# Kernel tuning notes

Hardware: AMD Instinct MI355X
Metric: run time of the kernel (lower is better)

Reference implementation:

```python
import jax, jax.numpy as jnp
import numpy as np

B, C, L, O = 32, 256, 336, 96
K, NLAYERS, DFF = 4, 2, 1024
EPS = 1e-5


def setup_inputs() -> dict:
    key = jax.random.key(0)
    ks = jax.random.split(key, 10)
    s1 = 1.0 / np.sqrt(L)
    s2 = 1.0 / np.sqrt(DFF)
    return {
        "x": jax.random.normal(ks[0], (B, C, L), dtype=jnp.float32),
        "rev_w": jnp.ones((C,), dtype=jnp.float32),
        "rev_b": jnp.zeros((C,), dtype=jnp.float32),
        "W1": jax.random.normal(ks[1], (K, NLAYERS, L, DFF), dtype=jnp.float32) * s1,
        "b1": jnp.zeros((K, NLAYERS, DFF), dtype=jnp.float32),
        "W2": jax.random.normal(ks[2], (K, NLAYERS, DFF, L), dtype=jnp.float32) * s2,
        "b2": jnp.zeros((K, NLAYERS, L), dtype=jnp.float32),
        "Wh": jax.random.normal(ks[3], (K, L, O), dtype=jnp.float32) * s1,
        "bh": jnp.zeros((K, O), dtype=jnp.float32),
        "assign": jax.random.randint(ks[4], (C,), 0, K, dtype=jnp.int32),
    }


def reference(x, rev_w, rev_b, W1, b1, W2, b2, Wh, bh, assign):
    # RevIN norm over the time axis, per instance and per channel. x: [B,C,L]
    mean = jnp.mean(x, axis=-1, keepdims=True)
    std = jnp.sqrt(jnp.var(x, axis=-1, keepdims=True) + EPS)
    xn = (x - mean) / std * rev_w[None, :, None] + rev_b[None, :, None]

    n_clusters = Wh.shape[0]
    n_layers = W1.shape[1]
    out = jnp.zeros(x.shape[:2] + (Wh.shape[-1],), dtype=x.dtype)  # [B,C,O]
    for k in range(n_clusters):
        z = xn  # [B,C,L] time-mixing MLP stack shared across channels
        for l in range(n_layers):
            h = jax.nn.relu(jnp.einsum('bcl,ld->bcd', z, W1[k, l]) + b1[k, l])
            z = z + jnp.einsum('bcd,dl->bcl', h, W2[k, l]) + b2[k, l]
        y = jnp.einsum('bcl,lo->bco', z, Wh[k]) + bh[k]  # [B,C,O]
        out = jnp.where((assign == k)[None, :, None], y, out)

    # RevIN denorm, then transpose to [B, out_len, C]
    out = (out - rev_b[None, :, None]) / rev_w[None, :, None] * std + mean
    return jnp.transpose(out, (0, 2, 1))
```

## Files before the change

kernel.cpp:

```cpp
#include <hip/hip_runtime.h>
#include <math.h>


typedef unsigned short u16;
typedef unsigned int u32;
typedef unsigned long long u64;

constexpr int B = 32, C = 256, L = 336, O = 96, K = 4, NL = 2, DFF = 1024;
constexpr int TM = 32;
constexpr int NTILES = (B * C) / TM;
constexpr int LP = 352;
constexpr int KS1 = LP / 32;
constexpr int KS2 = DFF / 32;
constexpr int NT2 = LP / 16;
constexpr int NTH = O / 16;
constexpr int ZBS = 360;
constexpr int HS = 1032;

constexpr int W1FRAGS = (DFF / 16) * KS1 * 64;
constexpr int W2FRAGS = NT2 * KS2 * 64;
constexpr int WHFRAGS = NTH * KS1 * 64;
constexpr int NW1 = W1FRAGS * K * NL;
constexpr int NW2 = W2FRAGS * K * NL;

typedef __bf16 bf16x8 __attribute__((ext_vector_type(8)));
typedef float f32x4 __attribute__((ext_vector_type(4)));

__device__ __forceinline__ u16 f2bf(float f) {
  union { float f; u32 u; } v;
  v.f = f;
  u32 r = v.u + 0x7fffu + ((v.u >> 16) & 1u);
  return (u16)(r >> 16);
}
__device__ __forceinline__ float bf2f(u16 h) {
  union { u32 u; float f; } v;
  v.u = ((u32)h) << 16;
  return v.f;
}
__device__ __forceinline__ u32 pack2(float a, float b) {
  return (u32)f2bf(a) | ((u32)f2bf(b) << 16);
}

__global__ __launch_bounds__(256) void build_tables(
    const int* __restrict__ assign, int* __restrict__ meta) {
  __shared__ int wcnt[4][K];
  __shared__ int pre[4][K];
  __shared__ int cofs[K + 1];
  const int tid = threadIdx.x;
  const int w = tid >> 6, lane = tid & 63;
  const int a = assign[tid];
  const u64 below = (1ull << lane) - 1ull;
  int myrank = 0;
#pragma unroll
  for (int k = 0; k < K; ++k) {
    const u64 m = __ballot(a == k);
    if (a == k) myrank = (int)__popcll(m & below);
    if (lane == 0) wcnt[w][k] = (int)__popcll(m);
  }
  __syncthreads();
  if (tid == 0) {
    int tot[K];
    for (int k = 0; k < K; ++k) {
      int s = 0;
      for (int ww = 0; ww < 4; ++ww) {
        pre[ww][k] = s;
        s += wcnt[ww][k];
      }
      tot[k] = s;
    }
    cofs[0] = 0;
    for (int k = 0; k < K; ++k) cofs[k + 1] = cofs[k] + tot[k];
    for (int k = 0; k <= K; ++k) meta[512 + k] = cofs[k];
  }
  __syncthreads();
  const int pos = cofs[a] + pre[w][a] + myrank;
  meta[256 + pos] = tid;
  int k = 0;
  while (k < K - 1 && tid >= cofs[k + 1]) ++k;
  meta[tid] = (k << 16) | ((tid - cofs[k]) * TM);
}


__global__ __launch_bounds__(256) void repack_w1(const float* __restrict__ W1,
                                                 u16* __restrict__ wbuf) {
  __shared__ u16 sm[32][516];
  const int tid = threadIdx.x;
  const int wid = tid >> 6, lane = tid & 63;
  const int dh = blockIdx.x & 1;
  const int ks = (blockIdx.x >> 1) % 11;
  const int kl = blockIdx.x / 22;
  for (int rr = 0; rr < 8; ++rr) {
    const int r = wid * 8 + rr;
    const int l = ks * 32 + r;
#pragma unroll
    for (int h = 0; h < 2; ++h) {
      const int c = h * 256 + lane * 4;
      float4 v = make_float4(0.f, 0.f, 0.f, 0.f);
      if (l < L)
        v = *(const float4*)(W1 + ((size_t)kl * L + l) * DFF + dh * 512 + c);
      uint2 p;
      p.x = pack2(v.x, v.y);
      p.y = pack2(v.z, v.w);
      *(uint2*)&sm[r][c] = p;
    }
  }
  __syncthreads();
  const int q = lane >> 4, rm = lane & 15;
  for (int e = 0; e < 8; ++e) {
    const int ntl = wid * 8 + e;
    const int nt = dh * 32 + ntl;
    uint4 o;
    u32 w4[4];
#pragma unroll
    for (int jj = 0; jj < 4; ++jj) {
      const u16 a = sm[q * 8 + 2 * jj][ntl * 16 + rm];
      const u16 b = sm[q * 8 + 2 * jj + 1][ntl * 16 + rm];
      w4[jj] = (u32)a | ((u32)b << 16);
    }
    o.x = w4[0]; o.y = w4[1]; o.z = w4[2]; o.w = w4[3];
    *(uint4*)(wbuf + ((size_t)(kl * 64 + nt) * 11 + ks) * 512 + lane * 8) = o;
  }
}

__global__ __launch_bounds__(256) void repack_w2(const float* __restrict__ W2,
                                                 u16* __restrict__ wbuf) {
  __shared__ u16 sm[32][356];
  const int tid = threadIdx.x;
  const int wid = tid >> 6, lane = tid & 63;
  const int ks = blockIdx.x & 31;
  const int kl = blockIdx.x >> 5;
  for (int rr = 0; rr < 8; ++rr) {
    const int r = wid * 8 + rr;
    const float* row = W2 + ((size_t)kl * DFF + ks * 32 + r) * L;
    {
      const int c = lane * 4;
      const float4 v = *(const float4*)(row + c);
      uint2 p;
      p.x = pack2(v.x, v.y);
      p.y = pack2(v.z, v.w);
      *(uint2*)&sm[r][c] = p;
    }
    {
      const int c = 256 + lane * 4;
      if (c < 352) {
        float4 v = make_float4(0.f, 0.f, 0.f, 0.f);
        if (c < L) v = *(const float4*)(row + c);
        uint2 p;
        p.x = pack2(v.x, v.y);
        p.y = pack2(v.z, v.w);
        *(uint2*)&sm[r][c] = p;
      }
    }
  }
  __syncthreads();
  const int q = lane >> 4, rm = lane & 15;
  for (int nt = wid; nt < NT2; nt += 4) {
    u32 w4[4];
#pragma unroll
    for (int jj = 0; jj < 4; ++jj) {
      const u16 a = sm[q * 8 + 2 * jj][nt * 16 + rm];
      const u16 b = sm[q * 8 + 2 * jj + 1][nt * 16 + rm];
      w4[jj] = (u32)a | ((u32)b << 16);
    }
    uint4 o;
    o.x = w4[0]; o.y = w4[1]; o.z = w4[2]; o.w = w4[3];
    *(uint4*)(wbuf + (size_t)NW1 * 8 +
              ((size_t)(kl * 22 + nt) * 32 + ks) * 512 + lane * 8) = o;
  }
}

__global__ __launch_bounds__(256) void repack_wh(const float* __restrict__ Wh,
                                                 u16* __restrict__ wbuf) {
  __shared__ u16 sm[32][100];
  const int tid = threadIdx.x;
  const int wid = tid >> 6, lane = tid & 63;
  const int ks = blockIdx.x % 11;
  const int kk = blockIdx.x / 11;
  for (int rr = 0; rr < 8; ++rr) {
    const int r = wid * 8 + rr;
    const int l = ks * 32 + r;
    if (lane < 24) {
      const int c = lane * 4;
      float4 v = make_float4(0.f, 0.f, 0.f, 0.f);
      if (l < L) v = *(const float4*)(Wh + ((size_t)kk * L + l) * O + c);
      uint2 p;
      p.x = pack2(v.x, v.y);
      p.y = pack2(v.z, v.w);
      *(uint2*)&sm[r][c] = p;
    }
  }
  __syncthreads();
  const int q = lane >> 4, rm = lane & 15;
  for (int nt = wid; nt < NTH; nt += 4) {
    u32 w4[4];
#pragma unroll
    for (int jj = 0; jj < 4; ++jj) {
      const u16 a = sm[q * 8 + 2 * jj][nt * 16 + rm];
      const u16 b = sm[q * 8 + 2 * jj + 1][nt * 16 + rm];
      w4[jj] = (u32)a | ((u32)b << 16);
    }
    uint4 o;
    o.x = w4[0]; o.y = w4[1]; o.z = w4[2]; o.w = w4[3];
    *(uint4*)(wbuf + (size_t)(NW1 + NW2) * 8 +
              ((size_t)(kk * 6 + nt) * 11 + ks) * 512 + lane * 8) = o;
  }
}

__global__ __launch_bounds__(512, 2) void mlp_mfma(
    const float* __restrict__ x, const float* __restrict__ rev_w,
    const float* __restrict__ rev_b, const float* __restrict__ b1,
    const float* __restrict__ b2, const float* __restrict__ bh,
    const int* __restrict__ meta, const u16* __restrict__ wbuf,
    float* __restrict__ out) {
  __shared__ __align__(16) u16 zb[TM][ZBS];
  __shared__ __align__(16) u16 Hsh[TM][HS];
  __shared__ float s_mean[TM], s_std[TM], s_rw[TM], s_rb[TM];
  __shared__ int s_b[TM], s_c[TM];

  const int tid = threadIdx.x;
  const int wid = tid >> 6;
  const int lane = tid & 63;
  const int q = lane >> 4, rm = lane & 15;

  const int swz = (blockIdx.x & 7) * 32 + (blockIdx.x >> 3);
  const int info = meta[swz];
  const int kcl = info >> 16;
  const int rstart = info & 0xffff;
  const int cofs = meta[512 + kcl];
  const int cnt = meta[512 + kcl + 1] - cofs;

  for (int i = 0; i < 4; ++i) {
    const int t = wid * 4 + i;
    const int ri = rstart + t;
    const int b = ri / cnt;
    const int c = meta[256 + cofs + (ri % cnt)];
    const float* xrow = x + (size_t)(b * C + c) * L;
    float v[6], s = 0.f, s2 = 0.f;
#pragma unroll
    for (int jj = 0; jj < 6; ++jj) {
      const int j = lane + jj * 64;
      v[jj] = (j < L) ? xrow[j] : 0.f;
      s += v[jj];
      s2 += v[jj] * v[jj];
    }
#pragma unroll
    for (int off = 32; off > 0; off >>= 1) {
      s += __shfl_down(s, off);
      s2 += __shfl_down(s2, off);
    }
    s = __shfl(s, 0);
    s2 = __shfl(s2, 0);
    const float mean = s * (1.f / L);
    const float var = s2 * (1.f / L) - mean * mean;
    const float stdv = sqrtf(var + 1e-5f);
    const float rstd = 1.f / stdv;
    const float rw = rev_w[c], rb_ = rev_b[c];
#pragma unroll
    for (int jj = 0; jj < 6; ++jj) {
      const int j = lane + jj * 64;
      if (j < L) zb[t][j] = f2bf((v[jj] - mean) * rstd * rw + rb_);
    }
    if (lane < LP - L) zb[t][L + lane] = 0;
    if (lane == 0) {
      s_mean[t] = mean;
      s_std[t] = stdv;
      s_rw[t] = rw;
      s_rb[t] = rb_;
      s_b[t] = b;
      s_c[t] = c;
    }
  }

  const u16* w1b = wbuf;
  const u16* w2b = wbuf + (size_t)NW1 * 8;
  const u16* whb = wbuf + (size_t)(NW1 + NW2) * 8;
  constexpr int TS1 = KS1 * 512;
  constexpr int TS2 = KS2 * 512;

  bf16x8 acur[8], anxt[8];
  {
    const u16* base =
        w1b + (size_t)(kcl * NL) * W1FRAGS * 8 + (size_t)(wid * 8) * TS1 + lane * 8;
#pragma unroll
    for (int t = 0; t < 8; ++t) {
      acur[t] = *(const bf16x8*)(base + (size_t)t * TS1);
      anxt[t] = *(const bf16x8*)(base + (size_t)t * TS1 + 512);
    }
  }
  __syncthreads();

  f32x4 zm[3][2];
#pragma unroll
  for (int t = 0; t < 3; ++t) {
    const int nt2 = wid + 8 * t;
#pragma unroll
    for (int rg = 0; rg < 2; ++rg) {
      if (nt2 < NT2) {
        const uint2 zw = *(const uint2*)&zb[rm + 16 * rg][nt2 * 16 + q * 4];
        zm[t][rg] = f32x4{bf2f((u16)zw.x), bf2f((u16)(zw.x >> 16)),
                          bf2f((u16)zw.y), bf2f((u16)(zw.y >> 16))};
      } else {
        zm[t][rg] = f32x4{0.f, 0.f, 0.f, 0.f};
      }
    }
  }

  for (int l = 0; l < NL; ++l) {
    const int kl = kcl * NL + l;
    const u16* W1f = w1b + (size_t)kl * W1FRAGS * 8;
    const u16* W2f = w2b + (size_t)kl * W2FRAGS * 8;
    const float* b1p = b1 + kl * DFF;
    const float* b2p = b2 + kl * L;
    const u16* base1 = W1f + (size_t)(wid * 8) * TS1 + lane * 8;

    f32x4 acc[8][2];
#pragma unroll
    for (int t = 0; t < 8; ++t)
#pragma unroll
      for (int rg = 0; rg < 2; ++rg) acc[t][rg] = f32x4{0.f, 0.f, 0.f, 0.f};
#pragma unroll 2
    for (int ks = 0; ks < KS1; ++ks) {
      bf16x8 ause[8];
#pragma unroll
      for (int t = 0; t < 8; ++t) {
        ause[t] = acur[t];
        acur[t] = anxt[t];
      }
      if (ks + 2 < KS1) {
#pragma unroll
        for (int t = 0; t < 8; ++t)
          anxt[t] = *(const bf16x8*)(base1 + (size_t)t * TS1 + (ks + 2) * 512);
      }
      const bf16x8 zf0 = *(const bf16x8*)&zb[rm][ks * 32 + q * 8];
      const bf16x8 zf1 = *(const bf16x8*)&zb[rm + 16][ks * 32 + q * 8];
#pragma unroll
      for (int t = 0; t < 8; ++t) {
        acc[t][0] =
            __builtin_amdgcn_mfma_f32_16x16x32_bf16(ause[t], zf0, acc[t][0], 0, 0, 0);
        acc[t][1] =
            __builtin_amdgcn_mfma_f32_16x16x32_bf16(ause[t], zf1, acc[t][1], 0, 0, 0);
      }
    }
#pragma unroll
    for (int t = 0; t < 8; ++t) {
      const int nt = wid * 8 + t;
      const float4 bq = *(const float4*)(b1p + nt * 16 + q * 4);
#pragma unroll
      for (int rg = 0; rg < 2; ++rg) {
        uint2 hw;
        hw.x = pack2(fmaxf(acc[t][rg][0] + bq.x, 0.f),
                     fmaxf(acc[t][rg][1] + bq.y, 0.f));
        hw.y = pack2(fmaxf(acc[t][rg][2] + bq.z, 0.f),
                     fmaxf(acc[t][rg][3] + bq.w, 0.f));
        *(uint2*)&Hsh[rm + 16 * rg][nt * 16 + q * 4] = hw;
      }
    }

    const u16* base2 = W2f + lane * 8;
    bf16x8 wq0[3], wq1[3], wq2[3];
#pragma unroll
    for (int t = 0; t < 3; ++t) {
      const int nt2 = wid + 8 * t;
      if (nt2 < NT2) {
        wq0[t] = *(const bf16x8*)(base2 + (size_t)nt2 * TS2);
        wq1[t] = *(const bf16x8*)(base2 + (size_t)nt2 * TS2 + 512);
        wq2[t] = *(const bf16x8*)(base2 + (size_t)nt2 * TS2 + 1024);
      }
    }
    __syncthreads();

#pragma unroll 2
    for (int ks = 0; ks < KS2; ++ks) {
      bf16x8 wuse[3];
#pragma unroll
      for (int t = 0; t < 3; ++t) {
        wuse[t] = wq0[t];
        wq0[t] = wq1[t];
        wq1[t] = wq2[t];
      }
      if (ks + 3 < KS2) {
#pragma unroll
        for (int t = 0; t < 3; ++t) {
          const int nt2 = wid + 8 * t;
          if (nt2 < NT2)
            wq2[t] = *(const bf16x8*)(base2 + (size_t)nt2 * TS2 + (ks + 3) * 512);
        }
      }
      const bf16x8 hf0 = *(const bf16x8*)&Hsh[rm][ks * 32 + q * 8];
      const bf16x8 hf1 = *(const bf16x8*)&Hsh[rm + 16][ks * 32 + q * 8];
#pragma unroll
      for (int t = 0; t < 3; ++t) {
        if (wid + 8 * t < NT2) {
          zm[t][0] =
              __builtin_amdgcn_mfma_f32_16x16x32_bf16(wuse[t], hf0, zm[t][0], 0, 0, 0);
          zm[t][1] =
              __builtin_amdgcn_mfma_f32_16x16x32_bf16(wuse[t], hf1, zm[t][1], 0, 0, 0);
        }
      }
    }

#pragma unroll
    for (int t = 0; t < 3; ++t) {
      const int nt2 = wid + 8 * t;
      if (nt2 < NT2) {
        const int lc = nt2 * 16 + q * 4;
        if (lc < L) {
          const float4 bq = *(const float4*)(b2p + lc);
          zm[t][0][0] += bq.x; zm[t][0][1] += bq.y;
          zm[t][0][2] += bq.z; zm[t][0][3] += bq.w;
          zm[t][1][0] += bq.x; zm[t][1][1] += bq.y;
          zm[t][1][2] += bq.z; zm[t][1][3] += bq.w;
        }
#pragma unroll
        for (int rg = 0; rg < 2; ++rg) {
          uint2 zw;
          zw.x = pack2(zm[t][rg][0], zm[t][rg][1]);
          zw.y = pack2(zm[t][rg][2], zm[t][rg][3]);
          *(uint2*)&zb[rm + 16 * rg][lc] = zw;
        }
      }
    }

    if (l + 1 < NL) {
      const u16* nb = w1b + (size_t)(kl + 1) * W1FRAGS * 8 +
                      (size_t)(wid * 8) * TS1 + lane * 8;
#pragma unroll
      for (int t = 0; t < 8; ++t) {
        acur[t] = *(const bf16x8*)(nb + (size_t)t * TS1);
        anxt[t] = *(const bf16x8*)(nb + (size_t)t * TS1 + 512);
      }
    }
    __syncthreads();
  }

  if (wid < NTH) {
    const u16* Whf =
        whb + (size_t)kcl * WHFRAGS * 8 + (size_t)wid * TS1 + lane * 8;
    f32x4 acc0 = {0.f, 0.f, 0.f, 0.f}, acc1 = {0.f, 0.f, 0.f, 0.f};
    for (int ks = 0; ks < KS1; ++ks) {
      const bf16x8 af = *(const bf16x8*)(Whf + ks * 512);
      const bf16x8 zf0 = *(const bf16x8*)&zb[rm][ks * 32 + q * 8];
      const bf16x8 zf1 = *(const bf16x8*)&zb[rm + 16][ks * 32 + q * 8];
      acc0 = __builtin_amdgcn_mfma_f32_16x16x32_bf16(af, zf0, acc0, 0, 0, 0);
      acc1 = __builtin_amdgcn_mfma_f32_16x16x32_bf16(af, zf1, acc1, 0, 0, 0);
    }
    const float4 bq = *(const float4*)(bh + kcl * O + wid * 16 + q * 4);
    const float bqa[4] = {bq.x, bq.y, bq.z, bq.w};
#pragma unroll
    for (int rg = 0; rg < 2; ++rg) {
      const int row = rm + 16 * rg;
      const float mean = s_mean[row], stdv = s_std[row];
      const float rw = s_rw[row], rb_ = s_rb[row];
      const int ob = s_b[row], oc = s_c[row];
      const f32x4 acc = rg ? acc1 : acc0;
#pragma unroll
      for (int gg = 0; gg < 4; ++gg) {
        const int o = wid * 16 + q * 4 + gg;
        const float y = acc[gg] + bqa[gg];
        out[((size_t)ob * O + o) * C + oc] = (y - rb_) / rw * stdv + mean;
      }
    }
  }
}

extern "C" void kernel_launch(void* const* d_in, const int* in_sizes, int n_in,
                              void* d_out, int out_size, void* d_ws,
                              size_t ws_size, hipStream_t stream) {
  const float* x = (const float*)d_in[0];
  const float* rev_w = (const float*)d_in[1];
  const float* rev_b = (const float*)d_in[2];
  const float* W1 = (const float*)d_in[3];
  const float* b1 = (const float*)d_in[4];
  const float* W2 = (const float*)d_in[5];
  const float* b2 = (const float*)d_in[6];
  const float* Wh = (const float*)d_in[7];
  const float* bh = (const float*)d_in[8];
  const int* assign = (const int*)d_in[9];
  float* out = (float*)d_out;

  int* meta = (int*)d_ws;
  u16* wbuf = (u16*)((char*)d_ws + 4096);

  build_tables<<<1, 256, 0, stream>>>(assign, meta);
  repack_w1<<<K * NL * 11 * 2, 256, 0, stream>>>(W1, wbuf);
  repack_w2<<<K * NL * 32, 256, 0, stream>>>(W2, wbuf);
  repack_wh<<<K * 11, 256, 0, stream>>>(Wh, wbuf);
  mlp_mfma<<<NTILES, 512, 0, stream>>>(x, rev_w, rev_b, b1, b2, bh, meta, wbuf,
                                       out);
}
```

Baseline: 177.8 us.

## Merge prep kernels into one launch and double workgroup to 1024 threads

Folds the table-building kernel and the three weight-repack kernels into a single prep kernel that dispatches on block index, removing three launch overheads. The main MLP kernel now uses 16 waves per workgroup instead of 8. Each wave owns half as many W1 column tiles and at most two W2 output tiles, which cuts per-thread register use and raises parallelism per tile. The trade-offs are more barrier participants, a launch bound of (1024,4) that may not match what actually fits per CU, and some waves left idle in the W2 and head stages.

After: 168.6 us. 5.2% less time.

```diff
diff --git a/kernel.cpp b/kernel.cpp
--- a/kernel.cpp
+++ b/kernel.cpp
@@ -22,6 +22,7 @@
 constexpr int WHFRAGS = NTH * KS1 * 64;
 constexpr int NW1 = W1FRAGS * K * NL;
 constexpr int NW2 = W2FRAGS * K * NL;
+constexpr int NPREP = 176 + 256 + 44 + 1;
 
 typedef __bf16 bf16x8 __attribute__((ext_vector_type(8)));
 typedef float f32x4 __attribute__((ext_vector_type(4)));
@@ -41,172 +42,162 @@
   return (u32)f2bf(a) | ((u32)f2bf(b) << 16);
 }
 
-__global__ __launch_bounds__(256) void build_tables(
-    const int* __restrict__ assign, int* __restrict__ meta) {
-  __shared__ int wcnt[4][K];
-  __shared__ int pre[4][K];
-  __shared__ int cofs[K + 1];
-  const int tid = threadIdx.x;
-  const int w = tid >> 6, lane = tid & 63;
-  const int a = assign[tid];
-  const u64 below = (1ull << lane) - 1ull;
-  int myrank = 0;
-#pragma unroll
-  for (int k = 0; k < K; ++k) {
-    const u64 m = __ballot(a == k);
-    if (a == k) myrank = (int)__popcll(m & below);
-    if (lane == 0) wcnt[w][k] = (int)__popcll(m);
-  }
-  __syncthreads();
-  if (tid == 0) {
-    int tot[K];
-    for (int k = 0; k < K; ++k) {
-      int s = 0;
-      for (int ww = 0; ww < 4; ++ww) {
-        pre[ww][k] = s;
-        s += wcnt[ww][k];
-      }
-      tot[k] = s;
-    }
-    cofs[0] = 0;
-    for (int k = 0; k < K; ++k) cofs[k + 1] = cofs[k] + tot[k];
-    for (int k = 0; k <= K; ++k) meta[512 + k] = cofs[k];
-  }
-  __syncthreads();
-  const int pos = cofs[a] + pre[w][a] + myrank;
-  meta[256 + pos] = tid;
-  int k = 0;
-  while (k < K - 1 && tid >= cofs[k + 1]) ++k;
-  meta[tid] = (k << 16) | ((tid - cofs[k]) * TM);
-}
-
-
-__global__ __launch_bounds__(256) void repack_w1(const float* __restrict__ W1,
-                                                 u16* __restrict__ wbuf) {
+__global__ __launch_bounds__(256) void prep(const int* __restrict__ assign,
+                                            const float* __restrict__ W1,
+                                            const float* __restrict__ W2,
+                                            const float* __restrict__ Wh,
+                                            int* __restrict__ meta,
+                                            u16* __restrict__ wbuf) {
   __shared__ u16 sm[32][516];
+  const int bid = blockIdx.x;
   const int tid = threadIdx.x;
   const int wid = tid >> 6, lane = tid & 63;
-  const int dh = blockIdx.x & 1;
-  const int ks = (blockIdx.x >> 1) % 11;
-  const int kl = blockIdx.x / 22;
-  for (int rr = 0; rr < 8; ++rr) {
-    const int r = wid * 8 + rr;
-    const int l = ks * 32 + r;
-#pragma unroll
-    for (int h = 0; h < 2; ++h) {
-      const int c = h * 256 + lane * 4;
-      float4 v = make_float4(0.f, 0.f, 0.f, 0.f);
-      if (l < L)
-        v = *(const float4*)(W1 + ((size_t)kl * L + l) * DFF + dh * 512 + c);
-      uint2 p;
-      p.x = pack2(v.x, v.y);
-      p.y = pack2(v.z, v.w);
-      *(uint2*)&sm[r][c] = p;
-    }
-  }
-  __syncthreads();
   const int q = lane >> 4, rm = lane & 15;
-  for (int e = 0; e < 8; ++e) {
-    const int ntl = wid * 8 + e;
-    const int nt = dh * 32 + ntl;
-    uint4 o;
-    u32 w4[4];
-#pragma unroll
-    for (int jj = 0; jj < 4; ++jj) {
-      const u16 a = sm[q * 8 + 2 * jj][ntl * 16 + rm];
-      const u16 b = sm[q * 8 + 2 * jj + 1][ntl * 16 + rm];
-      w4[jj] = (u32)a | ((u32)b << 16);
-    }
-    o.x = w4[0]; o.y = w4[1]; o.z = w4[2]; o.w = w4[3];
-    *(uint4*)(wbuf + ((size_t)(kl * 64 + nt) * 11 + ks) * 512 + lane * 8) = o;
-  }
-}
-
-__global__ __launch_bounds__(256) void repack_w2(const float* __restrict__ W2,
-                                                 u16* __restrict__ wbuf) {
-  __shared__ u16 sm[32][356];
-  const int tid = threadIdx.x;
-  const int wid = tid >> 6, lane = tid & 63;
-  const int ks = blockIdx.x & 31;
-  const int kl = blockIdx.x >> 5;
-  for (int rr = 0; rr < 8; ++rr) {
-    const int r = wid * 8 + rr;
-    const float* row = W2 + ((size_t)kl * DFF + ks * 32 + r) * L;
-    {
-      const int c = lane * 4;
-      const float4 v = *(const float4*)(row + c);
-      uint2 p;
-      p.x = pack2(v.x, v.y);
-      p.y = pack2(v.z, v.w);
-      *(uint2*)&sm[r][c] = p;
-    }
-    {
-      const int c = 256 + lane * 4;
-      if (c < 352) {
+
+  if (bid < 176) {
+    const int dh = bid & 1;
+    const int ks = (bid >> 1) % 11;
+    const int kl = bid / 22;
+    for (int rr = 0; rr < 8; ++rr) {
+      const int r = wid * 8 + rr;
+      const int l = ks * 32 + r;
+#pragma unroll
+      for (int h = 0; h < 2; ++h) {
+        const int c = h * 256 + lane * 4;
         float4 v = make_float4(0.f, 0.f, 0.f, 0.f);
-        if (c < L) v = *(const float4*)(row + c);
+        if (l < L)
+          v = *(const float4*)(W1 + ((size_t)kl * L + l) * DFF + dh * 512 + c);
         uint2 p;
         p.x = pack2(v.x, v.y);
         p.y = pack2(v.z, v.w);
         *(uint2*)&sm[r][c] = p;
       }
     }
-  }
-  __syncthreads();
-  const int q = lane >> 4, rm = lane & 15;
-  for (int nt = wid; nt < NT2; nt += 4) {
-    u32 w4[4];
-#pragma unroll
-    for (int jj = 0; jj < 4; ++jj) {
-      const u16 a = sm[q * 8 + 2 * jj][nt * 16 + rm];
-      const u16 b = sm[q * 8 + 2 * jj + 1][nt * 16 + rm];
-      w4[jj] = (u32)a | ((u32)b << 16);
-    }
-    uint4 o;
-    o.x = w4[0]; o.y = w4[1]; o.z = w4[2]; o.w = w4[3];
-    *(uint4*)(wbuf + (size_t)NW1 * 8 +
-              ((size_t)(kl * 22 + nt) * 32 + ks) * 512 + lane * 8) = o;
-  }
-}
-
-__global__ __launch_bounds__(256) void repack_wh(const float* __restrict__ Wh,
-                                                 u16* __restrict__ wbuf) {
-  __shared__ u16 sm[32][100];
-  const int tid = threadIdx.x;
-  const int wid = tid >> 6, lane = tid & 63;
-  const int ks = blockIdx.x % 11;
-  const int kk = blockIdx.x / 11;
-  for (int rr = 0; rr < 8; ++rr) {
-    const int r = wid * 8 + rr;
-    const int l = ks * 32 + r;
-    if (lane < 24) {
-      const int c = lane * 4;
-      float4 v = make_float4(0.f, 0.f, 0.f, 0.f);
-      if (l < L) v = *(const float4*)(Wh + ((size_t)kk * L + l) * O + c);
-      uint2 p;
-      p.x = pack2(v.x, v.y);
-      p.y = pack2(v.z, v.w);
-      *(uint2*)&sm[r][c] = p;
-    }
-  }
-  __syncthreads();
-  const int q = lane >> 4, rm = lane & 15;
-  for (int nt = wid; nt < NTH; nt += 4) {
-    u32 w4[4];
-#pragma unroll
-    for (int jj = 0; jj < 4; ++jj) {
-      const u16 a = sm[q * 8 + 2 * jj][nt * 16 + rm];
-      const u16 b = sm[q * 8 + 2 * jj + 1][nt * 16 + rm];
-      w4[jj] = (u32)a | ((u32)b << 16);
-    }
-    uint4 o;
-    o.x = w4[0]; o.y = w4[1]; o.z = w4[2]; o.w = w4[3];
-    *(uint4*)(wbuf + (size_t)(NW1 + NW2) * 8 +
-              ((size_t)(kk * 6 + nt) * 11 + ks) * 512 + lane * 8) = o;
-  }
-}
-
-__global__ __launch_bounds__(512, 2) void mlp_mfma(
+    __syncthreads();
+    for (int e = 0; e < 8; ++e) {
+      const int ntl = wid * 8 + e;
+      const int nt = dh * 32 + ntl;
+      u32 w4[4];
+#pragma unroll
+      for (int jj = 0; jj < 4; ++jj) {
+        const u16 a = sm[q * 8 + 2 * jj][ntl * 16 + rm];
+        const u16 b = sm[q * 8 + 2 * jj + 1][ntl * 16 + rm];
+        w4[jj] = (u32)a | ((u32)b << 16);
+      }
+      uint4 o;
+      o.x = w4[0]; o.y = w4[1]; o.z = w4[2]; o.w = w4[3];
+      *(uint4*)(wbuf + ((size_t)(kl * 64 + nt) * 11 + ks) * 512 + lane * 8) = o;
+    }
+  } else if (bid < 432) {
+    const int b2i = bid - 176;
+    const int ks = b2i & 31;
+    const int kl = b2i >> 5;
+    for (int rr = 0; rr < 8; ++rr) {
+      const int r = wid * 8 + rr;
+      const float* row = W2 + ((size_t)kl * DFF + ks * 32 + r) * L;
+      {
+        const int c = lane * 4;
+        const float4 v = *(const float4*)(row + c);
+        uint2 p;
+        p.x = pack2(v.x, v.y);
+        p.y = pack2(v.z, v.w);
+        *(uint2*)&sm[r][c] = p;
+      }
+      {
+        const int c = 256 + lane * 4;
+        if (c < 352) {
+          float4 v = make_float4(0.f, 0.f, 0.f, 0.f);
+          if (c < L) v = *(const float4*)(row + c);
+          uint2 p;
+          p.x = pack2(v.x, v.y);
+          p.y = pack2(v.z, v.w);
+          *(uint2*)&sm[r][c] = p;
+        }
+      }
+    }
+    __syncthreads();
+    for (int nt = wid; nt < NT2; nt += 4) {
+      u32 w4[4];
+#pragma unroll
+      for (int jj = 0; jj < 4; ++jj) {
+        const u16 a = sm[q * 8 + 2 * jj][nt * 16 + rm];
+        const u16 b = sm[q * 8 + 2 * jj + 1][nt * 16 + rm];
+        w4[jj] = (u32)a | ((u32)b << 16);
+      }
+      uint4 o;
+      o.x = w4[0]; o.y = w4[1]; o.z = w4[2]; o.w = w4[3];
+      *(uint4*)(wbuf + (size_t)NW1 * 8 +
+                ((size_t)(kl * 22 + nt) * 32 + ks) * 512 + lane * 8) = o;
+    }
+  } else if (bid < 476) {
+    const int b3i = bid - 432;
+    const int ks = b3i % 11;
+    const int kk = b3i / 11;
+    for (int rr = 0; rr < 8; ++rr) {
+      const int r = wid * 8 + rr;
+      const int l = ks * 32 + r;
+      if (lane < 24) {
+        const int c = lane * 4;
+        float4 v = make_float4(0.f, 0.f, 0.f, 0.f);
+        if (l < L) v = *(const float4*)(Wh + ((size_t)kk * L + l) * O + c);
+        uint2 p;
+        p.x = pack2(v.x, v.y);
+        p.y = pack2(v.z, v.w);
+        *(uint2*)&sm[r][c] = p;
+      }
+    }
+    __syncthreads();
+    for (int nt = wid; nt < NTH; nt += 4) {
+      u32 w4[4];
+#pragma unroll
+      for (int jj = 0; jj < 4; ++jj) {
+        const u16 a = sm[q * 8 + 2 * jj][nt * 16 + rm];
+        const u16 b = sm[q * 8 + 2 * jj + 1][nt * 16 + rm];
+        w4[jj] = (u32)a | ((u32)b << 16);
+      }
+      uint4 o;
+      o.x = w4[0]; o.y = w4[1]; o.z = w4[2]; o.w = w4[3];
+      *(uint4*)(wbuf + (size_t)(NW1 + NW2) * 8 +
+                ((size_t)(kk * 6 + nt) * 11 + ks) * 512 + lane * 8) = o;
+    }
+  } else {
+    __shared__ int wcnt[4][K];
+    __shared__ int pre[4][K];
+    __shared__ int cofs[K + 1];
+    const int a = assign[tid];
+    const u64 below = (1ull << lane) - 1ull;
+    int myrank = 0;
+#pragma unroll
+    for (int k = 0; k < K; ++k) {
+      const u64 m = __ballot(a == k);
+      if (a == k) myrank = (int)__popcll(m & below);
+      if (lane == 0) wcnt[wid][k] = (int)__popcll(m);
+    }
+    __syncthreads();
+    if (tid == 0) {
+      int tot[K];
+      for (int k = 0; k < K; ++k) {
+        int s = 0;
+        for (int ww = 0; ww < 4; ++ww) {
+          pre[ww][k] = s;
+          s += wcnt[ww][k];
+        }
+        tot[k] = s;
+      }
+      cofs[0] = 0;
+      for (int k = 0; k < K; ++k) cofs[k + 1] = cofs[k] + tot[k];
+      for (int k = 0; k <= K; ++k) meta[512 + k] = cofs[k];
+    }
+    __syncthreads();
+    const int pos = cofs[a] + pre[wid][a] + myrank;
+    meta[256 + pos] = tid;
+    int k = 0;
+    while (k < K - 1 && tid >= cofs[k + 1]) ++k;
+    meta[tid] = (k << 16) | ((tid - cofs[k]) * TM);
+  }
+}
+
+__global__ __launch_bounds__(1024, 4) void mlp_mfma(
     const float* __restrict__ x, const float* __restrict__ rev_w,
     const float* __restrict__ rev_b, const float* __restrict__ b1,
     const float* __restrict__ b2, const float* __restrict__ bh,
@@ -229,8 +220,8 @@
   const int cofs = meta[512 + kcl];
   const int cnt = meta[512 + kcl + 1] - cofs;
 
-  for (int i = 0; i < 4; ++i) {
-    const int t = wid * 4 + i;
+  for (int i = 0; i < 2; ++i) {
+    const int t = wid * 2 + i;
     const int ri = rstart + t;
     const int b = ri / cnt;
     const int c = meta[256 + cofs + (ri % cnt)];
@@ -277,30 +268,30 @@
   constexpr int TS1 = KS1 * 512;
   constexpr int TS2 = KS2 * 512;
 
-  bf16x8 acur[8], anxt[8];
+  bf16x8 acur[4], anxt[4];
   {
-    const u16* base =
-        w1b + (size_t)(kcl * NL) * W1FRAGS * 8 + (size_t)(wid * 8) * TS1 + lane * 8;
-#pragma unroll
-    for (int t = 0; t < 8; ++t) {
+    const u16* base = w1b + (size_t)(kcl * NL) * W1FRAGS * 8 +
+                      (size_t)(wid * 4) * TS1 + lane * 8;
+#pragma unroll
+    for (int t = 0; t < 4; ++t) {
       acur[t] = *(const bf16x8*)(base + (size_t)t * TS1);
       anxt[t] = *(const bf16x8*)(base + (size_t)t * TS1 + 512);
     }
   }
   __syncthreads();
 
-  f32x4 zm[3][2];
-#pragma unroll
-  for (int t = 0; t < 3; ++t) {
-    const int nt2 = wid + 8 * t;
+  f32x4 zm[2][2];
+#pragma unroll
+  for (int tt = 0; tt < 2; ++tt) {
+    const int nt2 = wid + 16 * tt;
 #pragma unroll
     for (int rg = 0; rg < 2; ++rg) {
       if (nt2 < NT2) {
         const uint2 zw = *(const uint2*)&zb[rm + 16 * rg][nt2 * 16 + q * 4];
-        zm[t][rg] = f32x4{bf2f((u16)zw.x), bf2f((u16)(zw.x >> 16)),
-                          bf2f((u16)zw.y), bf2f((u16)(zw.y >> 16))};
+        zm[tt][rg] = f32x4{bf2f((u16)zw.x), bf2f((u16)(zw.x >> 16)),
+                           bf2f((u16)zw.y), bf2f((u16)(zw.y >> 16))};
       } else {
-        zm[t][rg] = f32x4{0.f, 0.f, 0.f, 0.f};
+        zm[tt][rg] = f32x4{0.f, 0.f, 0.f, 0.f};
       }
     }
   }
@@ -311,39 +302,39 @@
     const u16* W2f = w2b + (size_t)kl * W2FRAGS * 8;
     const float* b1p = b1 + kl * DFF;
     const float* b2p = b2 + kl * L;
-    const u16* base1 = W1f + (size_t)(wid * 8) * TS1 + lane * 8;
-
-    f32x4 acc[8][2];
-#pragma unroll
-    for (int t = 0; t < 8; ++t)
+    const u16* base1 = W1f + (size_t)(wid * 4) * TS1 + lane * 8;
+
+    f32x4 acc[4][2];
+#pragma unroll
+    for (int t = 0; t < 4; ++t)
 #pragma unroll
       for (int rg = 0; rg < 2; ++rg) acc[t][rg] = f32x4{0.f, 0.f, 0.f, 0.f};
 #pragma unroll 2
     for (int ks = 0; ks < KS1; ++ks) {
-      bf16x8 ause[8];
-#pragma unroll
-      for (int t = 0; t < 8; ++t) {
+      bf16x8 ause[4];
+#pragma unroll
+      for (int t = 0; t < 4; ++t) {
         ause[t] = acur[t];
         acur[t] = anxt[t];
       }
       if (ks + 2 < KS1) {
 #pragma unroll
-        for (int t = 0; t < 8; ++t)
+        for (int t = 0; t < 4; ++t)
           anxt[t] = *(const bf16x8*)(base1 + (size_t)t * TS1 + (ks + 2) * 512);
       }
       const bf16x8 zf0 = *(const bf16x8*)&zb[rm][ks * 32 + q * 8];
       const bf16x8 zf1 = *(const bf16x8*)&zb[rm + 16][ks * 32 + q * 8];
 #pragma unroll
-      for (int t = 0; t < 8; ++t) {
-        acc[t][0] =
-            __builtin_amdgcn_mfma_f32_16x16x32_bf16(ause[t], zf0, acc[t][0], 0, 0, 0);
-        acc[t][1] =
-            __builtin_amdgcn_mfma_f32_16x16x32_bf16(ause[t], zf1, acc[t][1], 0, 0, 0);
-      }
-    }
-#pragma unroll
-    for (int t = 0; t < 8; ++t) {
-      const int nt = wid * 8 + t;
+      for (int t = 0; t < 4; ++t) {
+        acc[t][0] = __builtin_amdgcn_mfma_f32_16x16x32_bf16(ause[t], zf0,
+                                                            acc[t][0], 0, 0, 0);
+        acc[t][1] = __builtin_amdgcn_mfma_f32_16x16x32_bf16(ause[t], zf1,
+                                                            acc[t][1], 0, 0, 0);
+      }
+    }
+#pragma unroll
+    for (int t = 0; t < 4; ++t) {
+      const int nt = wid * 4 + t;
       const float4 bq = *(const float4*)(b1p + nt * 16 + q * 4);
 #pragma unroll
       for (int rg = 0; rg < 2; ++rg) {
@@ -357,65 +348,66 @@
     }
 
     const u16* base2 = W2f + lane * 8;
-    bf16x8 wq0[3], wq1[3], wq2[3];
-#pragma unroll
-    for (int t = 0; t < 3; ++t) {
-      const int nt2 = wid + 8 * t;
+    bf16x8 wq0[2], wq1[2], wq2[2];
+#pragma unroll
+    for (int tt = 0; tt < 2; ++tt) {
+      const int nt2 = wid + 16 * tt;
       if (nt2 < NT2) {
-        wq0[t] = *(const bf16x8*)(base2 + (size_t)nt2 * TS2);
-        wq1[t] = *(const bf16x8*)(base2 + (size_t)nt2 * TS2 + 512);
-        wq2[t] = *(const bf16x8*)(base2 + (size_t)nt2 * TS2 + 1024);
+        wq0[tt] = *(const bf16x8*)(base2 + (size_t)nt2 * TS2);
+        wq1[tt] = *(const bf16x8*)(base2 + (size_t)nt2 * TS2 + 512);
+        wq2[tt] = *(const bf16x8*)(base2 + (size_t)nt2 * TS2 + 1024);
       }
     }
     __syncthreads();
 
 #pragma unroll 2
     for (int ks = 0; ks < KS2; ++ks) {
-      bf16x8 wuse[3];
-#pragma unroll
-      for (int t = 0; t < 3; ++t) {
-        wuse[t] = wq0[t];
-        wq0[t] = wq1[t];
-        wq1[t] = wq2[t];
+      bf16x8 wuse[2];
+#pragma unroll
+      for (int tt = 0; tt < 2; ++tt) {
+        wuse[tt] = wq0[tt];
+        wq0[tt] = wq1[tt];
+        wq1[tt] = wq2[tt];
       }
       if (ks + 3 < KS2) {
 #pragma unroll
-        for (int t = 0; t < 3; ++t) {
-          const int nt2 = wid + 8 * t;
+        for (int tt = 0; tt < 2; ++tt) {
+          const int nt2 = wid + 16 * tt;
           if (nt2 < NT2)
-            wq2[t] = *(const bf16x8*)(base2 + (size_t)nt2 * TS2 + (ks + 3) * 512);
+            wq2[tt] =
+                *(const bf16x8*)(base2 + (size_t)nt2 * TS2 + (ks + 3) * 512);
         }
       }
       const bf16x8 hf0 = *(const bf16x8*)&Hsh[rm][ks * 32 + q * 8];
       const bf16x8 hf1 = *(const bf16x8*)&Hsh[rm + 16][ks * 32 + q * 8];
 #pragma unroll
-      for (int t = 0; t < 3; ++t) {
-        if (wid + 8 * t < NT2) {
-          zm[t][0] =
-              __builtin_amdgcn_mfma_f32_16x16x32_bf16(wuse[t], hf0, zm[t][0], 0, 0, 0);
-          zm[t][1] =
-              __builtin_amdgcn_mfma_f32_16x16x32_bf16(wuse[t], hf1, zm[t][1], 0, 0, 0);
-        }
-      }
-    }
-
-#pragma unroll
-    for (int t = 0; t < 3; ++t) {
-      const int nt2 = wid + 8 * t;
+      for (int tt = 0; tt < 2; ++tt) {
+        if (wid + 16 * tt < NT2) {
+          zm[tt][0] = __builtin_amdgcn_mfma_f32_16x16x32_bf16(wuse[tt], hf0,
+                                                              zm[tt][0], 0, 0, 0);
+          zm[tt][1] = __builtin_amdgcn_mfma_f32_16x16x32_bf16(wuse[tt], hf1,
+                                                              zm[tt][1], 0, 0, 0);
+        }
+      }
+    }
+
+#pragma unroll
+    for (int tt = 0; tt < 2; ++tt) {
+      const int nt2 = wid + 16 * tt;
       if (nt2 < NT2) {
         const int lc = nt2 * 16 + q * 4;
         if (lc < L) {
           const float4 bq = *(const float4*)(b2p + lc);
-          zm[t][0][0] += bq.x; zm[t][0][1] += bq.y;
-          zm[t][0][2] += bq.z; zm[t][0][3] += bq.w;
-          zm[t][1][0] += bq.x; zm[t][1][1] += bq.y;
-          zm[t][1][2] += bq.z; zm[t][1][3] += bq.w;
+          zm[tt][0][0] += bq.x; zm[tt][0][1] += bq.y;
+          zm[tt][0][2] += bq.z; zm[tt][0][3] += bq.w;
+          zm[tt][1][0] += bq.x; zm[tt][1][1] += bq.y;
+          zm[tt][1][2] += bq.z; zm[tt][1][3] += bq.w;
         }
 #pragma unroll
         for (int rg = 0; rg < 2; ++rg) {
           uint2 zw;
-          zw.x = pack2(zm[t][rg][0], zm[t][rg][1]);
-          zw.y = pack2(zm[t][rg][2], zm[t][rg][3]);
+          zw.x = pack2(zm[tt][rg][0], zm[tt][rg][1]);
+          zw.y = pack2(zm[tt][rg][2], zm[tt][rg][3]);
           *(uint2*)&zb[rm + 16 * rg][lc] = zw;
         }
       }
@@ -423,9 +415,9 @@
 
     if (l + 1 < NL) {
       const u16* nb = w1b + (size_t)(kl + 1) * W1FRAGS * 8 +
-                      (size_t)(wid * 8) * TS1 + lane * 8;
-#pragma unroll
-      for (int t = 0; t < 8; ++t) {
+                      (size_t)(wid * 4) * TS1 + lane * 8;
+#pragma unroll
+      for (int t = 0; t < 4; ++t) {
         acur[t] = *(const bf16x8*)(nb + (size_t)t * TS1);
         anxt[t] = *(const bf16x8*)(nb + (size_t)t * TS1 + 512);
       }
@@ -481,10 +473,7 @@
   int* meta = (int*)d_ws;
   u16* wbuf = (u16*)((char*)d_ws + 4096);
 
-  build_tables<<<1, 256, 0, stream>>>(assign, meta);
-  repack_w1<<<K * NL * 11 * 2, 256, 0, stream>>>(W1, wbuf);
-  repack_w2<<<K * NL * 32, 256, 0, stream>>>(W2, wbuf);
-  repack_wh<<<K * 11, 256, 0, stream>>>(Wh, wbuf);
-  mlp_mfma<<<NTILES, 512, 0, stream>>>(x, rev_w, rev_b, b1, b2, bh, meta, wbuf,
-                                       out);
-}
+  prep<<<NPREP, 256, 0, stream>>>(assign, W1, W2, Wh, meta, wbuf);
+  mlp_mfma<<<NTILES, 1024, 0, stream>>>(x, rev_w, rev_b, b1, b2, bh, meta,
+                                        wbuf, out);
+}
```
